# Kernel optimization log

Measured on AMD Instinct MI355X. Metric: run time of the kernel, lower is better.

The kernel has to match this reference:

```python
import jax, jax.numpy as jnp
import numpy as np

N = 100000   # nodes
E = 1600000  # edges (avg degree 16)
D = 128      # embed_dim
H1, C1 = 8, 16   # gat1: heads=8, out=embed_dim//8=16, concat -> 128
C2 = 32          # gat2: heads=1, out=32
NEG_SLOPE = 0.2  # PyG GATConv default leaky relu slope


def _gat_layer(x, src, dst, W, a_src, a_dst, b, heads, ch, concat):
    """PyG-style GATConv (eval mode, add_self_loops already applied via src/dst)."""
    n = x.shape[0]
    h = (x @ W).reshape(n, heads, ch)                      # [N,H,C]
    alpha_s = jnp.einsum('nhc,hc->nh', h, a_src)           # [N,H]
    alpha_d = jnp.einsum('nhc,hc->nh', h, a_dst)           # [N,H]
    e = jax.nn.leaky_relu(alpha_s[src] + alpha_d[dst], NEG_SLOPE)  # [Etot,H]
    # segment softmax over incoming edges of each dst node
    m = jax.ops.segment_max(e, dst, num_segments=n)        # [N,H]
    ex = jnp.exp(e - m[dst])
    s = jax.ops.segment_sum(ex, dst, num_segments=n)       # [N,H]
    alpha = ex / (s[dst] + 1e-16)                          # [Etot,H]
    out = jax.ops.segment_sum(alpha[:, :, None] * h[src], dst, num_segments=n)  # [N,H,C]
    out = out.reshape(n, heads * ch) if concat else out.mean(axis=1)
    return out + b


def setup_inputs():
    key = jax.random.key(0)
    ks = jax.random.split(key, 12)
    x = jax.random.normal(ks[0], (N, D), dtype=jnp.float32)
    edge_index = jax.random.randint(ks[1], (2, E), 0, N, dtype=jnp.int64)
    sc = 0.1
    W1 = jax.random.normal(ks[2], (D, H1 * C1), jnp.float32) * sc
    a1_src = jax.random.normal(ks[3], (H1, C1), jnp.float32) * sc
    a1_dst = jax.random.normal(ks[4], (H1, C1), jnp.float32) * sc
    b1 = jnp.zeros((H1 * C1,), jnp.float32)
    W2 = jax.random.normal(ks[5], (H1 * C1, C2), jnp.float32) * sc
    a2_src = jax.random.normal(ks[6], (1, C2), jnp.float32) * sc
    a2_dst = jax.random.normal(ks[7], (1, C2), jnp.float32) * sc
    b2 = jnp.zeros((C2,), jnp.float32)
    Wh = jax.random.normal(ks[8], (C2, 1), jnp.float32) * sc
    bh = jnp.zeros((1,), jnp.float32)
    return {"x": x, "edge_index": edge_index,
            "W1": W1, "a1_src": a1_src, "a1_dst": a1_dst, "b1": b1,
            "W2": W2, "a2_src": a2_src, "a2_dst": a2_dst, "b2": b2,
            "Wh": Wh, "bh": bh}


def reference(x, edge_index, W1, a1_src, a1_dst, b1, W2, a2_src, a2_dst, b2, Wh, bh):
    n = x.shape[0]
    loops = jnp.arange(n, dtype=edge_index.dtype)
    src = jnp.concatenate([edge_index[0], loops])  # add_self_loops=True (PyG default)
    dst = jnp.concatenate([edge_index[1], loops])
    h = jax.nn.elu(_gat_layer(x, src, dst, W1, a1_src, a1_dst, b1, H1, C1, True))
    h = jax.nn.elu(_gat_layer(h, src, dst, W2, a2_src, a2_dst, b2, 1, C2, False))
    return h @ Wh + bh  # [N,1] ordinal head
```

## Files before the change

### kernel.cpp

```cpp
#include <hip/hip_runtime.h>
#include <hip/hip_bf16.h>
#include <stdint.h>
#include <stddef.h>

#define NEG_SLOPE 0.2f
#define XS 136

#define NBK   196
#define BWSH  9
#define BCAP  12288
#define NPREP 64

typedef __bf16 bf16x8 __attribute__((ext_vector_type(8)));
typedef float  f32x4  __attribute__((ext_vector_type(4)));

__device__ __forceinline__ float bf2f(__hip_bfloat16 b){ return __bfloat162float(b); }
__device__ __forceinline__ float lo_bf(unsigned u){ return __uint_as_float(u << 16); }
__device__ __forceinline__ float hi_bf(unsigned u){ return __uint_as_float(u & 0xffff0000u); }
__device__ __forceinline__ float lrelu(float u){ return fmaxf(u, NEG_SLOPE * u); }
__device__ __forceinline__ unsigned short f2bf(float f){
    unsigned u = __float_as_uint(f);
    return (unsigned short)((u + 0x7fffu + ((u >> 16) & 1u)) >> 16);
}
__device__ __forceinline__ float bfs2f(unsigned short s){ return __uint_as_float((unsigned)s << 16); }
__device__ __forceinline__ float ldraw(const void* p, int i, int isf){
    return isf ? ((const float*)p)[i] : bf2f(((const __hip_bfloat16*)p)[i]);
}

__global__ void detect_kernel(const unsigned* __restrict__ ei,
                              const unsigned* __restrict__ xw,
                              int* __restrict__ flags,
                              int* __restrict__ gcur){
    __shared__ int vote;
    const int t = threadIdx.x;
    if (t == 0) vote = 0;
    if (t < NBK) gcur[t] = t * BCAP;
    __syncthreads();
    if (t < 64){
        unsigned long long m = __ballot(ei[2*t + 1] != 0u);
        if (t == 0) flags[0] = (m == 0ull) ? 1 : 0;
    }
    {
        unsigned lo = xw[t] & 0xffffu;
        unsigned e  = (lo >> 7) & 0xffu;
        int pl = ((lo & 0x7fffu) == 0u || (e >= 100u && e <= 140u)) ? 1 : 0;
        atomicAdd(&vote, pl);
    }
    __syncthreads();
    if (t == 0) flags[1] = (vote < 128) ? 1 : 0;
}

#define WTS_TOTAL 20993
__global__ __launch_bounds__(256) void prep_scatter_kernel(
        const void* __restrict__ ei, const int* __restrict__ flags,
        int* __restrict__ gcur, unsigned* __restrict__ pairs, int E, int Et, int nsb,
        const void* W1, const void* W2, const void* a1s, const void* a1d,
        const void* b1, const void* a2s, const void* a2d, const void* b2,
        const void* Wh, const void* bh,
        float* __restrict__ w, unsigned short* __restrict__ w1x,
        unsigned short* __restrict__ w2x){
    const int t = threadIdx.x;
    if ((int)blockIdx.x < nsb){
        __shared__ int cnt[NBK], base[NBK];
        const int e0 = blockIdx.x * 4096;
        const int nE = min(4096, Et - e0);
        for (int i = t; i < NBK; i += 256) cnt[i] = 0;
        __syncthreads();
        const int is64 = flags[0];
        int2 sd[16];
        int  rk[16];
#pragma unroll
        for (int k = 0; k < 16; k++){
            int j = t + k * 256;
            if (j < nE){
                int e = e0 + j, s, d;
                if (e >= E){ s = e - E; d = s; }
                else if (is64){
                    const long long* p = (const long long*)ei;
                    s = (int)p[e]; d = (int)p[(size_t)E + e];
                } else {
                    const int* p = (const int*)ei;
                    s = p[e]; d = p[(size_t)E + e];
                }
                sd[k] = make_int2(s, d);
                rk[k] = atomicAdd(&cnt[d >> BWSH], 1);
            } else sd[k].y = -1;
        }
        __syncthreads();
        for (int b = t; b < NBK; b += 256)
            base[b] = cnt[b] ? atomicAdd(&gcur[b], cnt[b]) : 0;
        __syncthreads();
#pragma unroll
        for (int k = 0; k < 16; k++){
            if (sd[k].y >= 0){
                int b = sd[k].y >> BWSH;
                pairs[(size_t)base[b] + rk[k]] =
                    ((unsigned)sd[k].x << BWSH) | (unsigned)(sd[k].y & 511);
            }
        }
    } else {
        const int p   = blockIdx.x - nsb;
        const int tid = p * 256 + t;
        const int NT  = NPREP * 256;
        const int isf = flags[1];
        for (int i = tid; i < 513; i += NT){
            int gi = 20480 + i;
            const void* src; int off;
            if      (gi < 20608){ src = a1s; off = gi - 20480; }
            else if (gi < 20736){ src = a1d; off = gi - 20608; }
            else if (gi < 20864){ src = b1;  off = gi - 20736; }
            else if (gi < 20896){ src = a2s; off = gi - 20864; }
            else if (gi < 20928){ src = a2d; off = gi - 20896; }
            else if (gi < 20960){ src = b2;  off = gi - 20928; }
            else if (gi < 20992){ src = Wh;  off = gi - 20960; }
            else                { src = bh;  off = 0; }
            w[gi] = ldraw(src, off, isf);
        }
        for (int i = tid; i < 16384; i += NT){
            int c = i >> 7, k = i & 127;
            w1x[i] = f2bf(ldraw(W1, k*128 + c, isf));
        }
        for (int i = tid; i < 4096; i += NT){
            int c = i >> 7, k = i & 127;
            w2x[i] = f2bf(ldraw(W2, k*32 + c, isf));
        }
        for (int i = tid; i < 12*128; i += NT) w2x[36*128 + i] = 0;
        for (int i = tid; i < 1024; i += NT){
            int h = i >> 7, k = i & 127;
            float ss = 0.f, dd = 0.f;
#pragma unroll
            for (int j = 0; j < 16; j++){
                float hv = ldraw(W1, k*128 + h*16 + j, isf);
                ss += hv * ldraw(a1s, h*16 + j, isf);
                dd += hv * ldraw(a1d, h*16 + j, isf);
            }
            unsigned short sh = f2bf(ss), dh = f2bf(dd);
            w1x[(128+h)*128 + k] = sh;
            w1x[(136+h)*128 + k] = f2bf(ss - bfs2f(sh));
            w1x[(144+h)*128 + k] = dh;
            w1x[(152+h)*128 + k] = f2bf(dd - bfs2f(dh));
        }
        for (int k = tid; k < 128; k += NT){
            float ss = 0.f, dd = 0.f;
#pragma unroll
            for (int j = 0; j < 32; j++){
                float hv = ldraw(W2, k*32 + j, isf);
                ss += hv * ldraw(a2s, j, isf);
                dd += hv * ldraw(a2d, j, isf);
            }
            unsigned short sh = f2bf(ss), dh = f2bf(dd);
            w2x[32*128 + k] = sh;
            w2x[33*128 + k] = f2bf(ss - bfs2f(sh));
            w2x[34*128 + k] = dh;
            w2x[35*128 + k] = f2bf(dd - bfs2f(dh));
        }
    }
}

__global__ __launch_bounds__(256) void g1csr_kernel(
        const unsigned* __restrict__ pairs, const int* __restrict__ gcur,
        int* __restrict__ rowptr, int* __restrict__ csr_src, int Nn,
        const void* __restrict__ xv, const unsigned short* __restrict__ w1x,
        const int* __restrict__ flags, __hip_bfloat16* __restrict__ h1b,
        float* __restrict__ as1, float* __restrict__ ad1){
    __shared__ __align__(16) char smem[52224];
    const int t = threadIdx.x;
    if ((int)blockIdx.x < NBK){
        int* ssz   = (int*)smem;
        int* sscan = ssz + 256;
        int* cnt   = sscan + 256;
        int* sh    = cnt + 512;
        const int b = blockIdx.x;
        int v = (t < NBK) ? (gcur[t] - t * BCAP) : 0;
        ssz[t] = v; sscan[t] = v;
        __syncthreads();
        for (int off = 1; off < 256; off <<= 1){
            int x = (t >= off) ? sscan[t - off] : 0;
            __syncthreads();
            sscan[t] += x;
            __syncthreads();
        }
        const int sz = ssz[b];
        const int eb = (b == 0) ? 0 : sscan[b - 1];
        if (b == 0 && t == 0) rowptr[Nn] = sscan[NBK - 1];
        const unsigned* pp = pairs + (size_t)b * BCAP;
        cnt[t] = 0; cnt[t + 256] = 0;
        __syncthreads();
        for (int i = t; i < sz; i += 256) atomicAdd(&cnt[pp[i] & 511u], 1);
        __syncthreads();
        int l0 = 2*t, l1 = 2*t + 1;
        int s0 = cnt[l0], s1 = cnt[l1], ts = s0 + s1;
        sh[t] = ts; __syncthreads();
        for (int off = 1; off < 256; off <<= 1){
            int x = (t >= off) ? sh[t - off] : 0;
            __syncthreads();
            sh[t] += x;
            __syncthreads();
        }
        int excl = sh[t] - ts;
        __syncthreads();
        cnt[l0] = eb + excl;
        cnt[l1] = eb + excl + s0;
        int n0 = (b << BWSH) + l0, n1 = (b << BWSH) + l1;
        if (n0 < Nn) rowptr[n0] = cnt[l0];
        if (n1 < Nn) rowptr[n1] = cnt[l1];
        __syncthreads();
        for (int i = t; i < sz; i += 256){
            unsigned sd = pp[i];
            int pos = atomicAdd(&cnt[sd & 511u], 1);
            csr_src[pos] = (int)(sd >> BWSH);
        }
    } else {
        __bf16* xls = (__bf16*)smem;
        __bf16* wls = (__bf16*)(smem + 64 * XS * 2);
        const int row0 = ((int)blockIdx.x - NBK) * 64;
        const int n = Nn;

#pragma unroll
        for (int k = 0; k < 8; k++){
            int e = (t + k * 256) * 8;
            int c = e >> 7, kk = e & 127;
            *(uint4*)(&wls[c * XS + kk]) = *(const uint4*)(w1x + e);
        }
        if (row0 + 64 <= n){
            if (flags[1]){
                const float* xp = (const float*)xv + (size_t)row0 * 128;
#pragma unroll
                for (int k = 0; k < 8; k++){
                    int e = (t + k * 256) * 4;
                    int row = e >> 7, col = e & 127;
                    float4 vv = *(const float4*)(xp + e);
                    uint2 o;
                    o.x = (unsigned)f2bf(vv.x) | ((unsigned)f2bf(vv.y) << 16);
                    o.y = (unsigned)f2bf(vv.z) | ((unsigned)f2bf(vv.w) << 16);
                    *(uint2*)(&xls[row * XS + col]) = o;
                }
            } else {
                const unsigned short* xp = (const unsigned short*)xv + (size_t)row0 * 128;
#pragma unroll
                for (int k = 0; k < 4; k++){
                    int e = (t + k * 256) * 8;
                    int row = e >> 7, col = e & 127;
                    *(uint4*)(&xls[row * XS + col]) = *(const uint4*)(xp + e);
                }
            }
        } else {
            const int limit = (n - row0) * 128;
            if (flags[1]){
                const float* xp = (const float*)xv + (size_t)row0 * 128;
                for (int i = t; i < 64 * 128; i += 256){
                    float v = (i < limit) ? xp[i] : 0.f;
                    xls[(i >> 7) * XS + (i & 127)] = (__bf16)v;
                }
            } else {
                const unsigned short* xp = (const unsigned short*)xv + (size_t)row0 * 128;
                for (int i = t; i < 64 * 128; i += 256){
                    unsigned short v = (i < limit) ? xp[i] : (unsigned short)0;
                    ((unsigned short*)xls)[(i >> 7) * XS + (i & 127)] = v;
                }
            }
        }
        __syncthreads();

        const int w    = t >> 6;
        const int lane = t & 63;
        const int l15  = lane & 15;
        const int quad = lane >> 4;

        f32x4 acc[8] = {};
        f32x4 accS = {}, accD = {};
        const __bf16* xbase = &xls[(w * 16 + l15) * XS + quad * 8];
        const __bf16* wbase = &wls[l15 * XS + quad * 8];
        const unsigned short* vsrow = w1x + (128 + l15) * 128 + quad * 8;
        const unsigned short* vdrow = w1x + (144 + l15) * 128 + quad * 8;

#pragma unroll
        for (int ks = 0; ks < 4; ks++){
            bf16x8 af = *(const bf16x8*)(xbase + ks * 32);
#pragma unroll
            for (int tt = 0; tt < 8; tt++){
                bf16x8 bfr = *(const bf16x8*)(wbase + tt * 16 * XS + ks * 32);
                acc[tt] = __builtin_amdgcn_mfma_f32_16x16x32_bf16(af, bfr, acc[tt], 0, 0, 0);
            }
            bf16x8 bS = *(const bf16x8*)(vsrow + ks * 32);
            bf16x8 bD = *(const bf16x8*)(vdrow + ks * 32);
            accS = __builtin_amdgcn_mfma_f32_16x16x32_bf16(af, bS, accS, 0, 0, 0);
            accD = __builtin_amdgcn_mfma_f32_16x16x32_bf16(af, bD, accD, 0, 0, 0);
        }

#pragma unroll
        for (int tt = 0; tt < 8; tt++){
            int col = tt * 16 + l15;
#pragma unroll
            for (int r = 0; r < 4; r++){
                int row = row0 + w * 16 + quad * 4 + r;
                if (row < n) h1b[(size_t)row * 128 + col] = __float2bfloat16(acc[tt][r]);
            }
        }
#pragma unroll
        for (int r = 0; r < 4; r++){
            float vs = accS[r] + __shfl_xor(accS[r], 8);
            float vd = accD[r] + __shfl_xor(accD[r], 8);
            int row = row0 + w * 16 + quad * 4 + r;
            if (l15 < 8 && row < n){
                as1[(size_t)row * 8 + l15] = vs;
                ad1[(size_t)row * 8 + l15] = vd;
            }
        }
    }
}

__global__ __launch_bounds__(256) void gather1_kernel(const int* __restrict__ rowptr,
                                                      const int* __restrict__ csr_src,
                                                      const float* __restrict__ as1,
                                                      const float* __restrict__ ad1,
                                                      const unsigned* __restrict__ h1u,
                                                      const float* __restrict__ b1,
                                                      const unsigned short* __restrict__ w2x,
                                                      __hip_bfloat16* __restrict__ h2b,
                                                      float* __restrict__ as2,
                                                      float* __restrict__ ad2, int n){
    __shared__ __align__(16) unsigned short w2s[36 * XS];
    __shared__ __align__(16) unsigned als[4 * 64];
    const int t = threadIdx.x;
    for (int i = t; i < 576; i += 256){
        int e = i * 8, c = e >> 7, kk = e & 127;
        *(uint4*)(&w2s[c * XS + kk]) = *(const uint4*)(w2x + e);
    }
    const int wv   = t >> 6;
    const int wid  = blockIdx.x * 4 + wv;
    const int lane = t & 63;
    const int g    = lane >> 3;
    const int h    = lane & 7;
    int start = 0, end = 0;
    float adv = 0.f;
    if (wid < n){
        start = rowptr[wid]; end = rowptr[wid + 1];
        adv = ad1[(size_t)wid * 8 + h];
    }
    float den = 0.f;
    float num[16] = {0.f,0.f,0.f,0.f,0.f,0.f,0.f,0.f,
                     0.f,0.f,0.f,0.f,0.f,0.f,0.f,0.f};
    int j   = start + g;
    int src = (j < end) ? __builtin_nontemporal_load(csr_src + j) : -1;
    const int iters = (end - start + 7) >> 3;
#pragma unroll 2
    for (int it = 0; it < iters; ++it){
        const int jn   = j + 8;
        const int srcn = (jn < end) ? __builtin_nontemporal_load(csr_src + jn) : -1;
        if (src >= 0){
            const unsigned* hp = h1u + (size_t)src * 64 + h * 8;
            uint4 hv0 = *(const uint4*)(hp);
            uint4 hv1 = *(const uint4*)(hp + 4);
            float u = lrelu(as1[src * 8 + h] + adv);
            float w = __expf(u);
            den += w;
            num[0]  += w * lo_bf(hv0.x); num[1]  += w * hi_bf(hv0.x);
            num[2]  += w * lo_bf(hv0.y); num[3]  += w * hi_bf(hv0.y);
            num[4]  += w * lo_bf(hv0.z); num[5]  += w * hi_bf(hv0.z);
            num[6]  += w * lo_bf(hv0.w); num[7]  += w * hi_bf(hv0.w);
            num[8]  += w * lo_bf(hv1.x); num[9]  += w * hi_bf(hv1.x);
            num[10] += w * lo_bf(hv1.y); num[11] += w * hi_bf(hv1.y);
            num[12] += w * lo_bf(hv1.z); num[13] += w * hi_bf(hv1.z);
            num[14] += w * lo_bf(hv1.w); num[15] += w * hi_bf(hv1.w);
        }
        j = jn; src = srcn;
    }
    den += __shfl_xor(den, 8); den += __shfl_xor(den, 16); den += __shfl_xor(den, 32);
#pragma unroll
    for (int k = 0; k < 16; k++){
        num[k] += __shfl_xor(num[k], 8);
        num[k] += __shfl_xor(num[k], 16);
        num[k] += __shfl_xor(num[k], 32);
    }
    if (g == 0 && wid < n){
        const int ch0 = h * 16;
        float inv = 1.f / (den + 1e-16f);
        unsigned* ap = als + wv * 64 + h * 8;
#pragma unroll
        for (int m = 0; m < 8; m++){
            float r0 = num[2*m]   * inv + b1[ch0 + 2*m];
            float r1 = num[2*m+1] * inv + b1[ch0 + 2*m + 1];
            r0 = r0 > 0.f ? r0 : __expf(r0) - 1.f;
            r1 = r1 > 0.f ? r1 : __expf(r1) - 1.f;
            ap[m] = (unsigned)f2bf(r0) | ((unsigned)f2bf(r1) << 16);
        }
    }
    __syncthreads();
    const int col  = lane;
    const int nwid = blockIdx.x * 4 + wv;
    float dot = 0.f;
    if (col < 36 && nwid < n){
        const unsigned* av = als + wv * 64;
        const unsigned short* wr = &w2s[col * XS];
#pragma unroll
        for (int k = 0; k < 16; k++){
            uint4 a  = *(const uint4*)(av + k * 4);
            uint4 wq = *(const uint4*)(wr + k * 8);
            dot += lo_bf(a.x)*lo_bf(wq.x) + hi_bf(a.x)*hi_bf(wq.x);
            dot += lo_bf(a.y)*lo_bf(wq.y) + hi_bf(a.y)*hi_bf(wq.y);
            dot += lo_bf(a.z)*lo_bf(wq.z) + hi_bf(a.z)*hi_bf(wq.z);
            dot += lo_bf(a.w)*lo_bf(wq.w) + hi_bf(a.w)*hi_bf(wq.w);
        }
    }
    if (nwid < n){
        if (col < 32){
            h2b[(size_t)nwid * 32 + col] = __float2bfloat16(dot);
        } else if (col < 36){
            float s = dot + __shfl_xor(dot, 1);
            if (col == 32) as2[nwid] = s;
            if (col == 34) ad2[nwid] = s;
        }
    }
}

__global__ __launch_bounds__(256) void gather2_kernel(const int* __restrict__ rowptr,
                                                      const int* __restrict__ csr_src,
                                                      const float* __restrict__ as2,
                                                      const float* __restrict__ ad2,
                                                      const unsigned* __restrict__ h2u,
                                                      const float* __restrict__ b2,
                                                      const float* __restrict__ Wh,
                                                      const float* __restrict__ bh,
                                                      const int* __restrict__ flags,
                                                      void* __restrict__ out, int n){
    int wid = blockIdx.x * 4 + (threadIdx.x >> 6);
    if (wid >= n) return;
    const int lane = threadIdx.x & 63;
    const int g = lane >> 2;
    const int c = lane & 3;
    const int start = rowptr[wid], end = rowptr[wid + 1];
    const float adv = ad2[wid];
    float den = 0.f;
    float num[8] = {0.f,0.f,0.f,0.f,0.f,0.f,0.f,0.f};
    int j   = start + g;
    int src = (j < end) ? __builtin_nontemporal_load(csr_src + j) : -1;
    const int iters = (end - start + 15) >> 4;
#pragma unroll 2
    for (int it = 0; it < iters; ++it){
        const int jn   = j + 16;
        const int srcn = (jn < end) ? __builtin_nontemporal_load(csr_src + jn) : -1;
        if (src >= 0){
            uint4 hv = *(const uint4*)(h2u + (size_t)src * 16 + c * 4);
            float u = lrelu(as2[src] + adv);
            float w = __expf(u);
            den += w;
            num[0] += w * lo_bf(hv.x); num[1] += w * hi_bf(hv.x);
            num[2] += w * lo_bf(hv.y); num[3] += w * hi_bf(hv.y);
            num[4] += w * lo_bf(hv.z); num[5] += w * hi_bf(hv.z);
            num[6] += w * lo_bf(hv.w); num[7] += w * hi_bf(hv.w);
        }
        j = jn; src = srcn;
    }
    den += __shfl_xor(den, 4); den += __shfl_xor(den, 8);
    den += __shfl_xor(den, 16); den += __shfl_xor(den, 32);
#pragma unroll
    for (int k = 0; k < 8; k++){
        num[k] += __shfl_xor(num[k], 4);
        num[k] += __shfl_xor(num[k], 8);
        num[k] += __shfl_xor(num[k], 16);
        num[k] += __shfl_xor(num[k], 32);
    }
    float p = 0.f;
    if (g == 0){
        const int ch0 = c * 8;
        float inv = 1.f / (den + 1e-16f);
#pragma unroll
        for (int k = 0; k < 8; k++){
            float v = num[k] * inv + b2[ch0 + k];
            v = v > 0.f ? v : __expf(v) - 1.f;
            p += v * Wh[ch0 + k];
        }
    }
    p += __shfl_xor(p, 1); p += __shfl_xor(p, 2);
    if (lane == 0){
        float r = p + bh[0];
        if (flags[1]) ((float*)out)[wid] = r;
        else          ((__hip_bfloat16*)out)[wid] = __float2bfloat16(r);
    }
}

extern "C" void kernel_launch(void* const* d_in, const int* in_sizes, int n_in,
                              void* d_out, int out_size, void* d_ws, size_t ws_size,
                              hipStream_t stream){
    const void* x   = d_in[0];
    const void* ei  = d_in[1];

    const int Nn = in_sizes[0] / 128;
    const int Ee = in_sizes[1] / 2;
    const int Et = Ee + Nn;
    const int nsb = (Et + 4095) / 4096;

    char* ws = (char*)d_ws;
    auto al = [](size_t v){ return (v + 255) & ~(size_t)255; };
    size_t off = 0;
    int*      flags  = (int*)(ws + off);      off = al(off + 16);
    float*    wts    = (float*)(ws + off);    off = al(off + (size_t)WTS_TOTAL * 4);
    unsigned short* w1x = (unsigned short*)(ws + off); off = al(off + 160 * 128 * 2);
    unsigned short* w2x = (unsigned short*)(ws + off); off = al(off + 48 * 128 * 2);
    int*      gcur   = (int*)(ws + off);      off = al(off + (size_t)NBK * 4);
    int*      rowptr = (int*)(ws + off);      off = al(off + (size_t)(Nn + 1) * 4);
    int*      csrs   = (int*)(ws + off);      off = al(off + (size_t)Et * 4);
    unsigned* pairs  = (unsigned*)(ws + off); off = al(off + (size_t)NBK * BCAP * 4);
    __hip_bfloat16* h1b = (__hip_bfloat16*)(ws + off); off = al(off + (size_t)Nn * 128 * 2);
    float* as1  = (float*)(ws + off); off = al(off + (size_t)Nn * 8 * 4);
    float* ad1  = (float*)(ws + off); off = al(off + (size_t)Nn * 8 * 4);
    __hip_bfloat16* h2b = (__hip_bfloat16*)(ws + off); off = al(off + (size_t)Nn * 32 * 2);
    float* as2  = (float*)(ws + off); off = al(off + (size_t)Nn * 4);
    float* ad2  = (float*)(ws + off); off = al(off + (size_t)Nn * 4);

    float* b1f  = wts + 20736;
    float* b2f  = wts + 20928;
    float* Whf  = wts + 20960;
    float* bhf  = wts + 20992;

    detect_kernel<<<1, 256, 0, stream>>>((const unsigned*)ei, (const unsigned*)x, flags, gcur);

    prep_scatter_kernel<<<nsb + NPREP, 256, 0, stream>>>(ei, flags, gcur, pairs, Ee, Et, nsb,
        d_in[2], d_in[6], d_in[3], d_in[4], d_in[5], d_in[7], d_in[8], d_in[9],
        d_in[10], d_in[11], wts, w1x, w2x);

    g1csr_kernel<<<NBK + (Nn + 63) / 64, 256, 0, stream>>>(pairs, gcur, rowptr, csrs, Nn,
        x, w1x, flags, h1b, as1, ad1);

    gather1_kernel<<<(Nn + 3) / 4, 256, 0, stream>>>(rowptr, csrs, as1, ad1,
                                                     (const unsigned*)h1b, b1f,
                                                     w2x, h2b, as2, ad2, Nn);

    gather2_kernel<<<(Nn + 3) / 4, 256, 0, stream>>>(rowptr, csrs, as2, ad2,
                                                     (const unsigned*)h2b, b2f,
                                                     Whf, bhf, flags, d_out, Nn);
}
```

Measured before the change: 341.7 us.

## Stage bucketed edge pairs in LDS and use MFMA for layer-2 projection

```diff
diff --git a/kernel.cpp b/kernel.cpp
--- a/kernel.cpp
+++ b/kernel.cpp
@@ -34,7 +34,7 @@
     __shared__ int vote;
     const int t = threadIdx.x;
     if (t == 0) vote = 0;
-    if (t < NBK) gcur[t] = t * BCAP;
+    if (t < NBK) gcur[t] = 0;
     __syncthreads();
     if (t < 64){
         unsigned long long m = __ballot(ei[2*t + 1] != 0u);
@@ -61,12 +61,15 @@
         unsigned short* __restrict__ w2x){
     const int t = threadIdx.x;
     if ((int)blockIdx.x < nsb){
-        __shared__ int cnt[NBK], base[NBK];
+        __shared__ int cnt[256];
+        __shared__ int scn[256];
+        __shared__ int base[NBK];
+        __shared__ unsigned stage[4096];
+        cnt[t] = 0;
+        __syncthreads();
+        const int is64 = flags[0];
         const int e0 = blockIdx.x * 4096;
         const int nE = min(4096, Et - e0);
-        for (int i = t; i < NBK; i += 256) cnt[i] = 0;
-        __syncthreads();
-        const int is64 = flags[0];
         int2 sd[16];
         int  rk[16];
 #pragma unroll
@@ -87,16 +90,33 @@
             } else sd[k].y = -1;
         }
         __syncthreads();
-        for (int b = t; b < NBK; b += 256)
-            base[b] = cnt[b] ? atomicAdd(&gcur[b], cnt[b]) : 0;
+        int v = cnt[t];
+        scn[t] = v;
+        __syncthreads();
+        for (int off = 1; off < 256; off <<= 1){
+            int x = (t >= off) ? scn[t - off] : 0;
+            __syncthreads();
+            scn[t] += x;
+            __syncthreads();
+        }
+        if (t < NBK) base[t] = cnt[t] ? atomicAdd(&gcur[t], cnt[t]) : 0;
         __syncthreads();
 #pragma unroll
         for (int k = 0; k < 16; k++){
             if (sd[k].y >= 0){
                 int b = sd[k].y >> BWSH;
-                pairs[(size_t)base[b] + rk[k]] =
+                stage[(scn[b] - cnt[b]) + rk[k]] =
                     ((unsigned)sd[k].x << BWSH) | (unsigned)(sd[k].y & 511);
             }
+        }
+        __syncthreads();
+        const int wv = t >> 6, lane = t & 63;
+        for (int b = wv; b < NBK; b += 4){
+            const int c  = cnt[b];
+            const int sb = scn[b] - c;
+            unsigned* gp = pairs + (size_t)b * BCAP + base[b];
+            const unsigned* sp = stage + sb;
+            for (int i = lane; i < c; i += 64) gp[i] = sp[i];
         }
     } else {
         const int p   = blockIdx.x - nsb;
@@ -171,7 +191,7 @@
         int* cnt   = sscan + 256;
         int* sh    = cnt + 512;
         const int b = blockIdx.x;
-        int v = (t < NBK) ? (gcur[t] - t * BCAP) : 0;
+        int v = (t < NBK) ? gcur[t] : 0;
         ssz[t] = v; sscan[t] = v;
         __syncthreads();
         for (int off = 1; off < 256; off <<= 1){
@@ -320,13 +340,9 @@
                                                       __hip_bfloat16* __restrict__ h2b,
                                                       float* __restrict__ as2,
                                                       float* __restrict__ ad2, int n){
-    __shared__ __align__(16) unsigned short w2s[36 * XS];
-    __shared__ __align__(16) unsigned als[4 * 64];
+    __shared__ __align__(16) unsigned als[16 * 64];
     const int t = threadIdx.x;
-    for (int i = t; i < 576; i += 256){
-        int e = i * 8, c = e >> 7, kk = e & 127;
-        *(uint4*)(&w2s[c * XS + kk]) = *(const uint4*)(w2x + e);
-    }
+    als[t] = 0u; als[t + 256] = 0u; als[t + 512] = 0u; als[t + 768] = 0u;
     const int wv   = t >> 6;
     const int wid  = blockIdx.x * 4 + wv;
     const int lane = t & 63;
@@ -376,40 +392,53 @@
     if (g == 0 && wid < n){
         const int ch0 = h * 16;
         float inv = 1.f / (den + 1e-16f);
-        unsigned* ap = als + wv * 64 + h * 8;
+        unsigned op[8];
 #pragma unroll
         for (int m = 0; m < 8; m++){
             float r0 = num[2*m]   * inv + b1[ch0 + 2*m];
             float r1 = num[2*m+1] * inv + b1[ch0 + 2*m + 1];
             r0 = r0 > 0.f ? r0 : __expf(r0) - 1.f;
             r1 = r1 > 0.f ? r1 : __expf(r1) - 1.f;
-            ap[m] = (unsigned)f2bf(r0) | ((unsigned)f2bf(r1) << 16);
-        }
+            op[m] = (unsigned)f2bf(r0) | ((unsigned)f2bf(r1) << 16);
+        }
+        const int sw = (wv & 3) << 2;
+        unsigned* ap = als + wv * 64;
+        *(uint4*)(ap + ((h * 8)     ^ sw)) = make_uint4(op[0], op[1], op[2], op[3]);
+        *(uint4*)(ap + ((h * 8 + 4) ^ sw)) = make_uint4(op[4], op[5], op[6], op[7]);
     }
     __syncthreads();
-    const int col  = lane;
-    const int nwid = blockIdx.x * 4 + wv;
-    float dot = 0.f;
-    if (col < 36 && nwid < n){
-        const unsigned* av = als + wv * 64;
-        const unsigned short* wr = &w2s[col * XS];
-#pragma unroll
-        for (int k = 0; k < 16; k++){
-            uint4 a  = *(const uint4*)(av + k * 4);
-            uint4 wq = *(const uint4*)(wr + k * 8);
-            dot += lo_bf(a.x)*lo_bf(wq.x) + hi_bf(a.x)*hi_bf(wq.x);
-            dot += lo_bf(a.y)*lo_bf(wq.y) + hi_bf(a.y)*hi_bf(wq.y);
-            dot += lo_bf(a.z)*lo_bf(wq.z) + hi_bf(a.z)*hi_bf(wq.z);
-            dot += lo_bf(a.w)*lo_bf(wq.w) + hi_bf(a.w)*hi_bf(wq.w);
-        }
-    }
-    if (nwid < n){
-        if (col < 32){
-            h2b[(size_t)nwid * 32 + col] = __float2bfloat16(dot);
-        } else if (col < 36){
-            float s = dot + __shfl_xor(dot, 1);
-            if (col == 32) as2[nwid] = s;
-            if (col == 34) ad2[nwid] = s;
+    if (wv < 3){
+        const int l15  = lane & 15;
+        const int quad = lane >> 4;
+        const int swr  = (l15 & 3) << 2;
+        f32x4 acc = {};
+        const unsigned short* brow = w2x + (wv * 16 + l15) * 128 + quad * 8;
+#pragma unroll
+        for (int ks = 0; ks < 4; ks++){
+            const unsigned* ap = als + l15 * 64 + (((quad * 4) + ks * 16) ^ swr);
+            bf16x8 af = *(const bf16x8*)ap;
+            bf16x8 bfr = *(const bf16x8*)(brow + ks * 32);
+            acc = __builtin_amdgcn_mfma_f32_16x16x32_bf16(af, bfr, acc, 0, 0, 0);
+        }
+        if (wv < 2){
+            if (quad == 0){
+#pragma unroll
+                for (int r = 0; r < 4; r++){
+                    int node = blockIdx.x * 4 + r;
+                    if (node < n)
+                        h2b[(size_t)node * 32 + wv * 16 + l15] = __float2bfloat16(acc[r]);
+                }
+            }
+        } else {
+#pragma unroll
+            for (int r = 0; r < 4; r++){
+                float vE = acc[r] + __shfl_xor(acc[r], 1);
+                int node = blockIdx.x * 4 + r;
+                if (quad == 0 && node < n){
+                    if (l15 == 0) as2[node] = vE;
+                    if (l15 == 2) ad2[node] = vE;
+                }
+            }
         }
     }
 }
```

Result: faster. 308.0 us (-9.9%).
